# Performance work log

Hardware: AMD Instinct MI355X
Metric: run time of the kernel (lower is better)

## Reference

```python
import jax, jax.numpy as jnp
import numpy as np


def _gru_scan(xg, w_hh, b_hh, h0):
    """Scan a GRU (PyTorch gate order r,z,n) over time. xg: (T,B,3H) precomputed input projections."""
    def step(h, g):
        gh = h @ w_hh.T + b_hh
        i_r, i_z, i_n = jnp.split(g, 3, axis=-1)
        h_r, h_z, h_n = jnp.split(gh, 3, axis=-1)
        r = jax.nn.sigmoid(i_r + h_r)
        z = jax.nn.sigmoid(i_z + h_z)
        n = jnp.tanh(i_n + r * h_n)
        h_new = (1.0 - z) * n + z * h
        return h_new, h_new
    _, ys = jax.lax.scan(step, h0, xg)
    return ys  # (T, B, H)


def setup_inputs() -> dict:
    key = jax.random.key(0)
    ks = jax.random.split(key, 13)
    B, M, T = 64, 80, 2000
    C, H, K = 256, 256, 5
    s = 0.1
    return {
        "x": jax.random.normal(ks[0], (B, M, T), jnp.float32),
        "conv_w": jax.random.normal(ks[1], (C, M, K), jnp.float32) * s,
        "conv_b": jax.random.normal(ks[2], (C,), jnp.float32) * s,
        "w_ih_f": jax.random.normal(ks[3], (3 * H, C), jnp.float32) * s,
        "w_hh_f": jax.random.normal(ks[4], (3 * H, H), jnp.float32) * s,
        "b_ih_f": jax.random.normal(ks[5], (3 * H,), jnp.float32) * s,
        "b_hh_f": jax.random.normal(ks[6], (3 * H,), jnp.float32) * s,
        "w_ih_r": jax.random.normal(ks[7], (3 * H, C), jnp.float32) * s,
        "w_hh_r": jax.random.normal(ks[8], (3 * H, H), jnp.float32) * s,
        "b_ih_r": jax.random.normal(ks[9], (3 * H,), jnp.float32) * s,
        "b_hh_r": jax.random.normal(ks[10], (3 * H,), jnp.float32) * s,
        "clf_w": jax.random.normal(ks[11], (2, 2 * H), jnp.float32) * s,
        "clf_b": jax.random.normal(ks[12], (2,), jnp.float32) * s,
        "window_size": 100,
    }


def reference(x, conv_w, conv_b, w_ih_f, w_hh_f, b_ih_f, b_hh_f,
              w_ih_r, w_hh_r, b_ih_r, b_hh_r, clf_w, clf_b, window_size):
    # Streaming (inference_mode) branch of KWSNet, expressed incrementally:
    # per-step sliding-window conv == full valid conv; the 'bidirectional' GRU
    # with seq_len=1 per step and carried hidden == two independent GRUs both
    # scanned forward in time (one with the _reverse weight set).
    B = x.shape[0]
    K = conv_w.shape[-1]
    H = w_hh_f.shape[-1]
    # Conv1d valid + ReLU: (B, C, Tc), Tc = T - K + 1
    y = jax.lax.conv_general_dilated(x, conv_w, (1,), 'VALID',
                                     dimension_numbers=('NCH', 'OIH', 'NCH'))
    y = jax.nn.relu(y + conv_b[None, :, None])
    seq = jnp.transpose(y, (2, 0, 1))  # (Tc, B, C)
    h0 = jnp.zeros((B, H), seq.dtype)
    xg_f = seq @ w_ih_f.T + b_ih_f  # (Tc, B, 3H)
    xg_r = seq @ w_ih_r.T + b_ih_r
    enc = jnp.concatenate([
        _gru_scan(xg_f, w_hh_f, b_hh_f, h0),
        _gru_scan(xg_r, w_hh_r, b_hh_r, h0),
    ], axis=-1)  # (Tc, B, 2H)
    # Sliding mean over the last W encoder outputs (W = window_size - K + 1)
    W = window_size - K + 1
    cs = jnp.concatenate([jnp.zeros_like(enc[:1]), jnp.cumsum(enc, axis=0)], axis=0)
    means = (cs[W:] - cs[:-W]) / W  # (Tout, B, 2H), Tout = T - window_size + 1
    out = means @ clf_w.T + clf_b  # (Tout, B, 2)
    # torch stacks per-step (1, B, 2) outputs -> (Tout, 1, B, 2)
    return out[:, None, :, :]
```

## Files before the change

### kernel.cpp

```cpp
#include <hip/hip_runtime.h>
#include <hip/hip_bf16.h>


#define TT    2000
#define TC    1996
#define NB    64
#define MCH   80
#define NN    1536
#define TOUT  1901
#define TCH   126
#define NCHK  16
#define NRG   9
#define CROWS (TCH * NB)

typedef _Float16 h8_t __attribute__((ext_vector_type(8)));
typedef float    f4_t __attribute__((ext_vector_type(4)));

#define WQSCALE 254.0f
#define INV8    (1.0f / (254.0f * 127.0f))

#define OFF_SEQC ((size_t)0)
#define OFF_XG   ((size_t)8257536)
#define OFF_WT   ((size_t)57802752)
#define OFF_WCAT ((size_t)58212352)
#define OFF_HST  ((size_t)58998784)
#define OFF_WQ   ((size_t)59129856)
#define OFF_PS2  ((size_t)59523072)

__global__ void prep_kernel(const float* __restrict__ conv_w,
                            const float* __restrict__ wihf,
                            const float* __restrict__ wihr,
                            const float* __restrict__ whhf,
                            const float* __restrict__ whhr,
                            float* __restrict__ wT,
                            _Float16* __restrict__ wcat,
                            unsigned* __restrict__ wq) {
    int idx = blockIdx.x * 256 + threadIdx.x;
    if (idx < 400 * 256) {
        int c = idx & 255, mk = idx >> 8;
        wT[idx] = conv_w[c * 400 + mk];
    }
    int i2 = idx - 400 * 256;
    if (i2 >= 0 && i2 < NN * 256) {
        int k = i2 & 255, n = i2 >> 8;
        float v = (n < 768) ? wihf[n * 256 + k] : wihr[(n - 768) * 256 + k];
        wcat[i2] = (_Float16)v;
    }
    int i4 = idx - (400 * 256 + NN * 256);
    if (i4 >= 0 && i4 < 2 * 3 * 256 * 64) {
        int r  = i4 & 255;
        int j  = (i4 >> 8) & 63;
        int dg = i4 >> 14;
        const float* whh = (dg >= 3) ? whhr : whhf;
        int g = (dg >= 3) ? dg - 3 : dg;
        const float* wp = whh + (size_t)(g * 256 + r) * 256 + 4 * j;
        unsigned v = 0;
#pragma unroll
        for (int kk = 0; kk < 4; ++kk) {
            float q = rintf(wp[kk] * WQSCALE);
            q = fminf(fmaxf(q, -127.f), 127.f);
            v |= ((unsigned)((int)q & 0xFF)) << (8 * kk);
        }
        wq[((size_t)dg * 256 + r) * 64 + j] = v;
    }
}

#define SD4(a, b, c) __builtin_amdgcn_sdot4((int)(a), (int)(b), (c), false)

__global__ __launch_bounds__(256)
void fat_kernel(
    int nscan, const _Float16* __restrict__ xg_s, const uint4* __restrict__ wq,
    const float* __restrict__ bhhf, const float* __restrict__ bhhr,
    const float* __restrict__ clfw, float* __restrict__ hstate,
    float* __restrict__ psum2, int t0s, int lens, int first,
    int nproj, const _Float16* __restrict__ seqc_p, const _Float16* __restrict__ wcat,
    const float* __restrict__ bihf, const float* __restrict__ bihr,
    _Float16* __restrict__ xg_p, int lenp,
    int nconv, const float* __restrict__ x, const float* __restrict__ wT,
    const float* __restrict__ conv_b, _Float16* __restrict__ seqc_c,
    int t0c, int lenc)
{
    __shared__ __align__(16) char smem[86016];
    int bid = blockIdx.x;
    int tid = threadIdx.x;

    if (bid < nscan) {
        int d = bid >> 6, b = bid & 63;
        int i = tid, lane = tid & 63, wv = tid >> 6;
        const float* bhh = d ? bhhr : bhhf;
        unsigned (*hq8)[64]  = (unsigned(*)[64])smem;
        float (*cwp)[4][2]   = (float(*)[4][2])(smem + 512);

        uint4 wa[16], wb[16], wc[16];
        {
            const uint4* pa = wq + ((size_t)(d * 3 + 0) * 256 + i) * 16;
            const uint4* pb = wq + ((size_t)(d * 3 + 1) * 256 + i) * 16;
            const uint4* pc = wq + ((size_t)(d * 3 + 2) * 256 + i) * 16;
#pragma unroll
            for (int k = 0; k < 16; ++k) { wa[k] = pa[k]; wb[k] = pb[k]; wc[k] = pc[k]; }
        }
        float bhr = bhh[i], bhz = bhh[256 + i], bhn = bhh[512 + i];
        float cw0 = clfw[d * 256 + i], cw1 = clfw[512 + d * 256 + i];
        float h = first ? 0.f : hstate[(size_t)bid * 256 + i];

        ((char*)&hq8[0][0])[i] = (char)(int)rintf(h * 127.f);
        __syncthreads();

        const _Float16* xgp = xg_s + (size_t)d * CROWS * 768 + (size_t)b * 768 + i;
        float xr = (float)xgp[0], xz = (float)xgp[256], xn = (float)xgp[512];
        xgp += (size_t)64 * 768;

        int cur = 0;
        for (int t = 0; t < lens; ++t) {
            float pxr = (float)xgp[0], pxz = (float)xgp[256], pxn = (float)xgp[512];
            xgp += (size_t)64 * 768;

            const uint4* hqp = (const uint4*)&hq8[cur][0];
            int i0 = 0, i1 = 0, i2 = 0;
#pragma unroll
            for (int k = 0; k < 16; ++k) {
                uint4 hv = hqp[k];
                i0 = SD4(wa[k].x, hv.x, i0); i0 = SD4(wa[k].y, hv.y, i0);
                i0 = SD4(wa[k].z, hv.z, i0); i0 = SD4(wa[k].w, hv.w, i0);
                i1 = SD4(wb[k].x, hv.x, i1); i1 = SD4(wb[k].y, hv.y, i1);
                i1 = SD4(wb[k].z, hv.z, i1); i1 = SD4(wb[k].w, hv.w, i1);
                i2 = SD4(wc[k].x, hv.x, i2); i2 = SD4(wc[k].y, hv.y, i2);
                i2 = SD4(wc[k].z, hv.z, i2); i2 = SD4(wc[k].w, hv.w, i2);
            }

            float hr = (float)i0 * INV8 + bhr;
            float hz = (float)i1 * INV8 + bhz;
            float hn = (float)i2 * INV8 + bhn;
            float rg = 1.f / (1.f + __expf(-(xr + hr)));
            float zg = 1.f / (1.f + __expf(-(xz + hz)));
            float xnr = xn + rg * hn;
            float nv = 1.f - 2.f / (__expf(2.f * xnr) + 1.f);
            h = (1.f - zg) * nv + zg * h;

            float s0 = cw0 * h, s1 = cw1 * h;
#pragma unroll
            for (int off = 32; off; off >>= 1) {
                s0 += __shfl_xor(s0, off, 64);
                s1 += __shfl_xor(s1, off, 64);
            }
            int nxt = cur ^ 1;
            ((char*)&hq8[nxt][0])[i] = (char)(int)rintf(h * 127.f);
            if (lane == 0) { cwp[nxt][wv][0] = s0; cwp[nxt][wv][1] = s1; }
            __syncthreads();
            if (i == 0) {
                float a0 = cwp[nxt][0][0] + cwp[nxt][1][0] + cwp[nxt][2][0] + cwp[nxt][3][0];
                float a1 = cwp[nxt][0][1] + cwp[nxt][1][1] + cwp[nxt][2][1] + cwp[nxt][3][1];
                float* pp = psum2 + (((size_t)d * TC + (t0s + t)) * 64 + b) * 2;
                pp[0] = a0; pp[1] = a1;
            }
            cur = nxt;
            xr = pxr; xz = pxz; xn = pxn;
        }
        hstate[(size_t)bid * 256 + i] = h;

    } else if (bid < nscan + nproj) {
        int pb = bid - nscan;
        int n0 = (pb % 12) * 128;
        int rg = pb / 12;
        int ntiles = lenp >> 1;
        _Float16 (*Bs)[264] = (_Float16(*)[264])smem;
        _Float16 (*As)[72]  = (_Float16(*)[72])(smem + 67584);
        int lane = tid & 63, wv = tid >> 6;
        int wr = wv >> 1, wcn = wv & 1;
        int fm = lane & 15, fq = lane >> 4;
        int r = tid >> 1, part = tid & 1;

        {
            const uint4* srcB = (const uint4*)&wcat[(size_t)(n0 + r) * 256 + part * 128];
            uint4* dstB = (uint4*)&Bs[r][part * 128];
#pragma unroll
            for (int q = 0; q < 16; ++q) dstB[q] = srcB[q];
        }

        for (int tIdx = rg; tIdx < ntiles; tIdx += NRG) {
            int row0 = tIdx * 128;
            f4_t acc[4][4];
#pragma unroll
            for (int mt = 0; mt < 4; ++mt)
#pragma unroll
                for (int nt = 0; nt < 4; ++nt) acc[mt][nt] = (f4_t){0.f, 0.f, 0.f, 0.f};

            for (int kc = 0; kc < 4; ++kc) {
                const uint4* srcA = (const uint4*)&seqc_p[(size_t)(row0 + r) * 256 + kc * 64 + part * 32];
                uint4* dstA = (uint4*)&As[r][part * 32];
                dstA[0] = srcA[0]; dstA[1] = srcA[1]; dstA[2] = srcA[2]; dstA[3] = srcA[3];
                __syncthreads();
#pragma unroll
                for (int ks = 0; ks < 64; ks += 32) {
                    h8_t af[4], bf[4];
#pragma unroll
                    for (int mt = 0; mt < 4; ++mt)
                        af[mt] = *(const h8_t*)&As[wr * 64 + mt * 16 + fm][ks + fq * 8];
#pragma unroll
                    for (int nt = 0; nt < 4; ++nt)
                        bf[nt] = *(const h8_t*)&Bs[wcn * 64 + nt * 16 + fm][kc * 64 + ks + fq * 8];
#pragma unroll
                    for (int mt = 0; mt < 4; ++mt)
#pragma unroll
                        for (int nt = 0; nt < 4; ++nt)
                            acc[mt][nt] = __builtin_amdgcn_mfma_f32_16x16x32_f16(
                                af[mt], bf[nt], acc[mt][nt], 0, 0, 0);
                }
                __syncthreads();
            }
#pragma unroll
            for (int nt = 0; nt < 4; ++nt) {
                int col = n0 + wcn * 64 + nt * 16 + fm;
                int d = (col < 768) ? 0 : 1;
                int j = col - d * 768;
                float bias = d ? bihr[j] : bihf[j];
                size_t obase = (size_t)d * CROWS * 768 + j;
#pragma unroll
                for (int mt = 0; mt < 4; ++mt) {
                    int row = row0 + wr * 64 + mt * 16 + fq * 4;
#pragma unroll
                    for (int rr = 0; rr < 4; ++rr)
                        xg_p[obase + (size_t)(row + rr) * 768] = (_Float16)(acc[mt][nt][rr] + bias);
                }
            }
        }

    } else {
        int cb = bid - nscan - nproj;
        int tile = cb >> 6;
        int b    = cb & 63;
        float (*xs)[68] = (float(*)[68])smem;
        for (int idx = tid; idx < MCH * 68; idx += 256) {
            int m = idx / 68, ii = idx - m * 68;
            int tt = t0c + tile * 64 + ii;
            xs[m][ii] = (tt < TT) ? x[(size_t)b * (MCH * TT) + m * TT + tt] : 0.f;
        }
        __syncthreads();
        int lane = tid & 63, tg = tid >> 6;
        float acc[4][16];
#pragma unroll
        for (int cq = 0; cq < 4; ++cq)
#pragma unroll
            for (int t = 0; t < 16; ++t) acc[cq][t] = 0.f;

        for (int m = 0; m < MCH; ++m) {
            float xr_[20];
#pragma unroll
            for (int q = 0; q < 5; ++q) {
                float4 v = *(const float4*)&xs[m][tg * 16 + q * 4];
                xr_[q * 4 + 0] = v.x; xr_[q * 4 + 1] = v.y;
                xr_[q * 4 + 2] = v.z; xr_[q * 4 + 3] = v.w;
            }
#pragma unroll
            for (int cq = 0; cq < 4; ++cq) {
                int c = lane + cq * 64;
                const float* wp = wT + (size_t)(m * 5) * 256 + c;
                float w0_ = wp[0], w1_ = wp[256], w2_ = wp[512], w3_ = wp[768], w4_ = wp[1024];
#pragma unroll
                for (int t = 0; t < 16; ++t)
                    acc[cq][t] += w0_ * xr_[t] + w1_ * xr_[t + 1] + w2_ * xr_[t + 2]
                                + w3_ * xr_[t + 3] + w4_ * xr_[t + 4];
            }
        }
#pragma unroll
        for (int cq = 0; cq < 4; ++cq) {
            int c = lane + cq * 64;
            float cb_ = conv_b[c];
            for (int t = 0; t < 16; ++t) {
                int tl = tile * 64 + tg * 16 + t;
                if (tl < lenc) {
                    float v = acc[cq][t] + cb_;
                    v = v > 0.f ? v : 0.f;
                    seqc_c[((size_t)tl * 64 + b) * 256 + c] = (_Float16)v;
                }
            }
        }
    }
}

__global__ void final_kernel(const float* __restrict__ psum2, const float* __restrict__ clf_b,
                             const int* __restrict__ win, float* __restrict__ out) {
    int idx = blockIdx.x * 256 + threadIdx.x;
    if (idx >= TOUT * 128) return;
    int c = idx & 1;
    int rem = idx >> 1;
    int b = rem & 63;
    int tau = rem >> 6;
    int W = win[0] - 5 + 1;
    const float* p0 = psum2;
    const float* p1 = psum2 + (size_t)TC * 64 * 2;
    float s = 0.f;
    for (int j = 0; j < W; ++j) {
        size_t o = ((size_t)(tau + j) * 64 + b) * 2 + c;
        s += p0[o] + p1[o];
    }
    out[idx] = s / (float)W + clf_b[c];
}

extern "C" void kernel_launch(void* const* d_in, const int* in_sizes, int n_in,
                              void* d_out, int out_size, void* d_ws, size_t ws_size,
                              hipStream_t stream) {
    const float* x      = (const float*)d_in[0];
    const float* conv_w = (const float*)d_in[1];
    const float* conv_b = (const float*)d_in[2];
    const float* w_ih_f = (const float*)d_in[3];
    const float* w_hh_f = (const float*)d_in[4];
    const float* b_ih_f = (const float*)d_in[5];
    const float* b_hh_f = (const float*)d_in[6];
    const float* w_ih_r = (const float*)d_in[7];
    const float* w_hh_r = (const float*)d_in[8];
    const float* b_ih_r = (const float*)d_in[9];
    const float* b_hh_r = (const float*)d_in[10];
    const float* clf_w  = (const float*)d_in[11];
    const float* clf_b  = (const float*)d_in[12];
    const int*   win    = (const int*)d_in[13];
    float* out = (float*)d_out;

    char* ws = (char*)d_ws;
    _Float16* seqc = (_Float16*)(ws + OFF_SEQC);
    _Float16* xg   = (_Float16*)(ws + OFF_XG);
    float*    wT   = (float*)(ws + OFF_WT);
    _Float16* wcat = (_Float16*)(ws + OFF_WCAT);
    float*    hst  = (float*)(ws + OFF_HST);
    const uint4* wqp = (const uint4*)(ws + OFF_WQ);
    unsigned* wq   = (unsigned*)(ws + OFF_WQ);
    float*    ps2  = (float*)(ws + OFF_PS2);

    const size_t XGP = (size_t)2 * CROWS * 768;
    const size_t SQP = (size_t)CROWS * 256;

    int prep_elems = 400 * 256 + NN * 256 + 2 * 3 * 256 * 64;
    prep_kernel<<<(prep_elems + 255) / 256, 256, 0, stream>>>(
        conv_w, w_ih_f, w_ih_r, w_hh_f, w_hh_r, wT, wcat, wq);

    auto lenk = [](int k) { return (k < NCHK - 1) ? TCH : (TC - (NCHK - 1) * TCH); };

    fat_kernel<<<128, 256, 0, stream>>>(
        0, xg, wqp, b_hh_f, b_hh_r, clf_w, hst, ps2, 0, 0, 0,
        0, seqc, wcat, b_ih_f, b_ih_r, xg, 0,
        128, x, wT, conv_b, seqc, 0, lenk(0));

    fat_kernel<<<12 * NRG + 128, 256, 0, stream>>>(
        0, xg, wqp, b_hh_f, b_hh_r, clf_w, hst, ps2, 0, 0, 0,
        12 * NRG, seqc, wcat, b_ih_f, b_ih_r, xg, lenk(0),
        128, x, wT, conv_b, seqc + SQP, TCH, lenk(1));

    for (int k = 0; k < NCHK; ++k) {
        int lens = lenk(k);
        int np = (k + 1 < NCHK) ? 12 * NRG : 0;
        int lp = (k + 1 < NCHK) ? lenk(k + 1) : 0;
        int nc = (k + 2 < NCHK) ? 128 : 0;
        fat_kernel<<<128 + np + nc, 256, 0, stream>>>(
            128, xg + (size_t)(k & 1) * XGP, wqp, b_hh_f, b_hh_r, clf_w, hst, ps2,
            k * TCH, lens, (k == 0) ? 1 : 0,
            np, seqc + (size_t)((k + 1) & 1) * SQP, wcat, b_ih_f, b_ih_r,
            xg + (size_t)((k + 1) & 1) * XGP, lp,
            nc, x, wT, conv_b, seqc + (size_t)(k & 1) * SQP,
            (k + 2) * TCH, (k + 2 < NCHK) ? lenk(k + 2) : 0);
    }

    final_kernel<<<(TOUT * 128 + 255) / 256, 256, 0, stream>>>(ps2, clf_b, win, out);
}
```

Measured before the change: 2.363 ms.

## Size time chunks from workspace budget and grid-stride conv tiles

```diff
diff --git a/kernel.cpp b/kernel.cpp
--- a/kernel.cpp
+++ b/kernel.cpp
@@ -8,24 +8,13 @@
 #define MCH   80
 #define NN    1536
 #define TOUT  1901
-#define TCH   126
-#define NCHK  16
 #define NRG   9
-#define CROWS (TCH * NB)
 
 typedef _Float16 h8_t __attribute__((ext_vector_type(8)));
 typedef float    f4_t __attribute__((ext_vector_type(4)));
 
 #define WQSCALE 254.0f
 #define INV8    (1.0f / (254.0f * 127.0f))
-
-#define OFF_SEQC ((size_t)0)
-#define OFF_XG   ((size_t)8257536)
-#define OFF_WT   ((size_t)57802752)
-#define OFF_WCAT ((size_t)58212352)
-#define OFF_HST  ((size_t)58998784)
-#define OFF_WQ   ((size_t)59129856)
-#define OFF_PS2  ((size_t)59523072)
 
 __global__ void prep_kernel(const float* __restrict__ conv_w,
                             const float* __restrict__ wihf,
@@ -69,6 +58,7 @@
 
 __global__ __launch_bounds__(256)
 void fat_kernel(
+    int crows,
     int nscan, const _Float16* __restrict__ xg_s, const uint4* __restrict__ wq,
     const float* __restrict__ bhhf, const float* __restrict__ bhhr,
     const float* __restrict__ clfw, float* __restrict__ hstate,
@@ -106,7 +96,7 @@
         ((char*)&hq8[0][0])[i] = (char)(int)rintf(h * 127.f);
         __syncthreads();
 
-        const _Float16* xgp = xg_s + (size_t)d * CROWS * 768 + (size_t)b * 768 + i;
+        const _Float16* xgp = xg_s + (size_t)d * crows * 768 + (size_t)b * 768 + i;
         float xr = (float)xgp[0], xz = (float)xgp[256], xn = (float)xgp[512];
         xgp += (size_t)64 * 768;
 
@@ -214,7 +204,7 @@
                 int d = (col < 768) ? 0 : 1;
                 int j = col - d * 768;
                 float bias = d ? bihr[j] : bihf[j];
-                size_t obase = (size_t)d * CROWS * 768 + j;
+                size_t obase = (size_t)d * crows * 768 + j;
 #pragma unroll
                 for (int mt = 0; mt < 4; ++mt) {
                     int row = row0 + wr * 64 + mt * 16 + fq * 4;
@@ -227,53 +217,57 @@
 
     } else {
         int cb = bid - nscan - nproj;
-        int tile = cb >> 6;
-        int b    = cb & 63;
+        int units = ((lenc + 63) >> 6) << 6;
         float (*xs)[68] = (float(*)[68])smem;
-        for (int idx = tid; idx < MCH * 68; idx += 256) {
-            int m = idx / 68, ii = idx - m * 68;
-            int tt = t0c + tile * 64 + ii;
-            xs[m][ii] = (tt < TT) ? x[(size_t)b * (MCH * TT) + m * TT + tt] : 0.f;
-        }
-        __syncthreads();
         int lane = tid & 63, tg = tid >> 6;
-        float acc[4][16];
-#pragma unroll
-        for (int cq = 0; cq < 4; ++cq)
-#pragma unroll
-            for (int t = 0; t < 16; ++t) acc[cq][t] = 0.f;
-
-        for (int m = 0; m < MCH; ++m) {
-            float xr_[20];
-#pragma unroll
-            for (int q = 0; q < 5; ++q) {
-                float4 v = *(const float4*)&xs[m][tg * 16 + q * 4];
-                xr_[q * 4 + 0] = v.x; xr_[q * 4 + 1] = v.y;
-                xr_[q * 4 + 2] = v.z; xr_[q * 4 + 3] = v.w;
+        for (int u = cb; u < units; u += nconv) {
+            int tile = u >> 6;
+            int b    = u & 63;
+            for (int idx = tid; idx < MCH * 68; idx += 256) {
+                int m = idx / 68, ii = idx - m * 68;
+                int tt = t0c + tile * 64 + ii;
+                xs[m][ii] = (tt < TT) ? x[(size_t)b * (MCH * TT) + m * TT + tt] : 0.f;
+            }
+            __syncthreads();
+            float acc[4][16];
+#pragma unroll
+            for (int cq = 0; cq < 4; ++cq)
+#pragma unroll
+                for (int t = 0; t < 16; ++t) acc[cq][t] = 0.f;
+
+            for (int m = 0; m < MCH; ++m) {
+                float xr_[20];
+#pragma unroll
+                for (int q = 0; q < 5; ++q) {
+                    float4 v = *(const float4*)&xs[m][tg * 16 + q * 4];
+                    xr_[q * 4 + 0] = v.x; xr_[q * 4 + 1] = v.y;
+                    xr_[q * 4 + 2] = v.z; xr_[q * 4 + 3] = v.w;
+                }
+#pragma unroll
+                for (int cq = 0; cq < 4; ++cq) {
+                    int c = lane + cq * 64;
+                    const float* wp = wT + (size_t)(m * 5) * 256 + c;
+                    float w0_ = wp[0], w1_ = wp[256], w2_ = wp[512], w3_ = wp[768], w4_ = wp[1024];
+#pragma unroll
+                    for (int t = 0; t < 16; ++t)
+                        acc[cq][t] += w0_ * xr_[t] + w1_ * xr_[t + 1] + w2_ * xr_[t + 2]
+                                    + w3_ * xr_[t + 3] + w4_ * xr_[t + 4];
+                }
             }
 #pragma unroll
             for (int cq = 0; cq < 4; ++cq) {
                 int c = lane + cq * 64;
-                const float* wp = wT + (size_t)(m * 5) * 256 + c;
-                float w0_ = wp[0], w1_ = wp[256], w2_ = wp[512], w3_ = wp[768], w4_ = wp[1024];
-#pragma unroll
-                for (int t = 0; t < 16; ++t)
-                    acc[cq][t] += w0_ * xr_[t] + w1_ * xr_[t + 1] + w2_ * xr_[t + 2]
-                                + w3_ * xr_[t + 3] + w4_ * xr_[t + 4];
-            }
-        }
-#pragma unroll
-        for (int cq = 0; cq < 4; ++cq) {
-            int c = lane + cq * 64;
-            float cb_ = conv_b[c];
-            for (int t = 0; t < 16; ++t) {
-                int tl = tile * 64 + tg * 16 + t;
-                if (tl < lenc) {
-                    float v = acc[cq][t] + cb_;
-                    v = v > 0.f ? v : 0.f;
-                    seqc_c[((size_t)tl * 64 + b) * 256 + c] = (_Float16)v;
-                }
-            }
+                float cb_ = conv_b[c];
+                for (int t = 0; t < 16; ++t) {
+                    int tl = tile * 64 + tg * 16 + t;
+                    if (tl < lenc) {
+                        float v = acc[cq][t] + cb_;
+                        v = v > 0.f ? v : 0.f;
+                        seqc_c[((size_t)tl * 64 + b) * 256 + c] = (_Float16)v;
+                    }
+                }
+            }
+            __syncthreads();
         }
     }
 }
@@ -316,47 +310,60 @@
     const int*   win    = (const int*)d_in[13];
     float* out = (float*)d_out;
 
+    const size_t FIXED_TAIL = 409600 + 786432 + 131072 + 393216 + 2043904;
+    size_t budget = (ws_size > FIXED_TAIL) ? (ws_size - FIXED_TAIL) : 0;
+    int tch = (int)(budget / 458752);
+    if (tch > 250) tch = 250;
+    if (tch < 64) tch = 64;
+    tch &= ~1;
+    int nchk = (TC + tch - 1) / tch;
+    int crows = tch * 64;
+
     char* ws = (char*)d_ws;
-    _Float16* seqc = (_Float16*)(ws + OFF_SEQC);
-    _Float16* xg   = (_Float16*)(ws + OFF_XG);
-    float*    wT   = (float*)(ws + OFF_WT);
-    _Float16* wcat = (_Float16*)(ws + OFF_WCAT);
-    float*    hst  = (float*)(ws + OFF_HST);
-    const uint4* wqp = (const uint4*)(ws + OFF_WQ);
-    unsigned* wq   = (unsigned*)(ws + OFF_WQ);
-    float*    ps2  = (float*)(ws + OFF_PS2);
-
-    const size_t XGP = (size_t)2 * CROWS * 768;
-    const size_t SQP = (size_t)CROWS * 256;
+    size_t off = 0;
+    _Float16* seqc = (_Float16*)(ws + off); off += (size_t)2 * crows * 256 * 2;
+    _Float16* xg   = (_Float16*)(ws + off); off += (size_t)2 * 2 * crows * 768 * 2;
+    float*    wT   = (float*)(ws + off);    off += 409600;
+    _Float16* wcat = (_Float16*)(ws + off); off += 786432;
+    float*    hst  = (float*)(ws + off);    off += 131072;
+    unsigned* wq   = (unsigned*)(ws + off);
+    const uint4* wqp = (const uint4*)(ws + off); off += 393216;
+    float*    ps2  = (float*)(ws + off);
+
+    const size_t XGP = (size_t)2 * crows * 768;
+    const size_t SQP = (size_t)crows * 256;
 
     int prep_elems = 400 * 256 + NN * 256 + 2 * 3 * 256 * 64;
     prep_kernel<<<(prep_elems + 255) / 256, 256, 0, stream>>>(
         conv_w, w_ih_f, w_ih_r, w_hh_f, w_hh_r, wT, wcat, wq);
 
-    auto lenk = [](int k) { return (k < NCHK - 1) ? TCH : (TC - (NCHK - 1) * TCH); };
+    auto lenk = [&](int k) { return (k < nchk - 1) ? tch : (TC - (nchk - 1) * tch); };
 
     fat_kernel<<<128, 256, 0, stream>>>(
+        crows,
         0, xg, wqp, b_hh_f, b_hh_r, clf_w, hst, ps2, 0, 0, 0,
         0, seqc, wcat, b_ih_f, b_ih_r, xg, 0,
         128, x, wT, conv_b, seqc, 0, lenk(0));
 
     fat_kernel<<<12 * NRG + 128, 256, 0, stream>>>(
+        crows,
         0, xg, wqp, b_hh_f, b_hh_r, clf_w, hst, ps2, 0, 0, 0,
         12 * NRG, seqc, wcat, b_ih_f, b_ih_r, xg, lenk(0),
-        128, x, wT, conv_b, seqc + SQP, TCH, lenk(1));
-
-    for (int k = 0; k < NCHK; ++k) {
+        128, x, wT, conv_b, seqc + SQP, tch, lenk(1));
+
+    for (int k = 0; k < nchk; ++k) {
         int lens = lenk(k);
-        int np = (k + 1 < NCHK) ? 12 * NRG : 0;
-        int lp = (k + 1 < NCHK) ? lenk(k + 1) : 0;
-        int nc = (k + 2 < NCHK) ? 128 : 0;
+        int np = (k + 1 < nchk) ? 12 * NRG : 0;
+        int lp = (k + 1 < nchk) ? lenk(k + 1) : 0;
+        int nc = (k + 2 < nchk) ? 128 : 0;
         fat_kernel<<<128 + np + nc, 256, 0, stream>>>(
+            crows,
             128, xg + (size_t)(k & 1) * XGP, wqp, b_hh_f, b_hh_r, clf_w, hst, ps2,
-            k * TCH, lens, (k == 0) ? 1 : 0,
+            k * tch, lens, (k == 0) ? 1 : 0,
             np, seqc + (size_t)((k + 1) & 1) * SQP, wcat, b_ih_f, b_ih_r,
             xg + (size_t)((k + 1) & 1) * XGP, lp,
             nc, x, wT, conv_b, seqc + (size_t)(k & 1) * SQP,
-            (k + 2) * TCH, (k + 2 < NCHK) ? lenk(k + 2) : 0);
+            (k + 2) * tch, (k + 2 < nchk) ? lenk(k + 2) : 0);
     }
 
     final_kernel<<<(TOUT * 128 + 255) / 256, 256, 0, stream>>>(ps2, clf_b, win, out);
```

Result: no change. 2.383 ms (+0.9%).

## Process two batch rows per GRU scan block and loop conv blocks

Applied to the files above, without the earlier changes.

```diff
diff --git a/kernel.cpp b/kernel.cpp
--- a/kernel.cpp
+++ b/kernel.cpp
@@ -85,11 +85,12 @@
     int tid = threadIdx.x;
 
     if (bid < nscan) {
-        int d = bid >> 6, b = bid & 63;
+        int d = bid >> 5, p = bid & 31;
+        int b0 = p * 2, b1 = p * 2 + 1;
         int i = tid, lane = tid & 63, wv = tid >> 6;
         const float* bhh = d ? bhhr : bhhf;
-        unsigned (*hq8)[64]  = (unsigned(*)[64])smem;
-        float (*cwp)[4][2]   = (float(*)[4][2])(smem + 512);
+        unsigned (*hq8)[2][64] = (unsigned(*)[2][64])smem;
+        float (*cwp)[4][2][2]  = (float(*)[4][2][2])(smem + 1024);
 
         uint4 wa[16], wb[16], wc[16];
         {
@@ -101,62 +102,93 @@
         }
         float bhr = bhh[i], bhz = bhh[256 + i], bhn = bhh[512 + i];
         float cw0 = clfw[d * 256 + i], cw1 = clfw[512 + d * 256 + i];
-        float h = first ? 0.f : hstate[(size_t)bid * 256 + i];
-
-        ((char*)&hq8[0][0])[i] = (char)(int)rintf(h * 127.f);
+        float h0 = first ? 0.f : hstate[(size_t)(d * 64 + b0) * 256 + i];
+        float h1 = first ? 0.f : hstate[(size_t)(d * 64 + b1) * 256 + i];
+
+        ((char*)&hq8[0][0][0])[i] = (char)(int)rintf(h0 * 127.f);
+        ((char*)&hq8[0][1][0])[i] = (char)(int)rintf(h1 * 127.f);
         __syncthreads();
 
-        const _Float16* xgp = xg_s + (size_t)d * CROWS * 768 + (size_t)b * 768 + i;
-        float xr = (float)xgp[0], xz = (float)xgp[256], xn = (float)xgp[512];
-        xgp += (size_t)64 * 768;
+        const _Float16* xgpA = xg_s + (size_t)d * CROWS * 768 + (size_t)b0 * 768 + i;
+        const _Float16* xgpB = xgpA + 768;
+        float xr0 = (float)xgpA[0], xz0 = (float)xgpA[256], xn0 = (float)xgpA[512];
+        float xr1 = (float)xgpB[0], xz1 = (float)xgpB[256], xn1 = (float)xgpB[512];
+        xgpA += (size_t)64 * 768; xgpB += (size_t)64 * 768;
 
         int cur = 0;
         for (int t = 0; t < lens; ++t) {
-            float pxr = (float)xgp[0], pxz = (float)xgp[256], pxn = (float)xgp[512];
-            xgp += (size_t)64 * 768;
-
-            const uint4* hqp = (const uint4*)&hq8[cur][0];
-            int i0 = 0, i1 = 0, i2 = 0;
+            float pr0 = (float)xgpA[0], pz0 = (float)xgpA[256], pn0 = (float)xgpA[512];
+            float pr1 = (float)xgpB[0], pz1 = (float)xgpB[256], pn1 = (float)xgpB[512];
+            xgpA += (size_t)64 * 768; xgpB += (size_t)64 * 768;
+
+            const uint4* hqpA = (const uint4*)&hq8[cur][0][0];
+            const uint4* hqpB = (const uint4*)&hq8[cur][1][0];
+            int i0a = 0, i1a = 0, i2a = 0, i0b = 0, i1b = 0, i2b = 0;
 #pragma unroll
             for (int k = 0; k < 16; ++k) {
-                uint4 hv = hqp[k];
-                i0 = SD4(wa[k].x, hv.x, i0); i0 = SD4(wa[k].y, hv.y, i0);
-                i0 = SD4(wa[k].z, hv.z, i0); i0 = SD4(wa[k].w, hv.w, i0);
-                i1 = SD4(wb[k].x, hv.x, i1); i1 = SD4(wb[k].y, hv.y, i1);
-                i1 = SD4(wb[k].z, hv.z, i1); i1 = SD4(wb[k].w, hv.w, i1);
-                i2 = SD4(wc[k].x, hv.x, i2); i2 = SD4(wc[k].y, hv.y, i2);
-                i2 = SD4(wc[k].z, hv.z, i2); i2 = SD4(wc[k].w, hv.w, i2);
-            }
-
-            float hr = (float)i0 * INV8 + bhr;
-            float hz = (float)i1 * INV8 + bhz;
-            float hn = (float)i2 * INV8 + bhn;
-            float rg = 1.f / (1.f + __expf(-(xr + hr)));
-            float zg = 1.f / (1.f + __expf(-(xz + hz)));
-            float xnr = xn + rg * hn;
-            float nv = 1.f - 2.f / (__expf(2.f * xnr) + 1.f);
-            h = (1.f - zg) * nv + zg * h;
-
-            float s0 = cw0 * h, s1 = cw1 * h;
+                uint4 hva = hqpA[k], hvb = hqpB[k];
+                i0a = SD4(wa[k].x, hva.x, i0a); i0a = SD4(wa[k].y, hva.y, i0a);
+                i0a = SD4(wa[k].z, hva.z, i0a); i0a = SD4(wa[k].w, hva.w, i0a);
+                i1a = SD4(wb[k].x, hva.x, i1a); i1a = SD4(wb[k].y, hva.y, i1a);
+                i1a = SD4(wb[k].z, hva.z, i1a); i1a = SD4(wb[k].w, hva.w, i1a);
+                i2a = SD4(wc[k].x, hva.x, i2a); i2a = SD4(wc[k].y, hva.y, i2a);
+                i2a = SD4(wc[k].z, hva.z, i2a); i2a = SD4(wc[k].w, hva.w, i2a);
+                i0b = SD4(wa[k].x, hvb.x, i0b); i0b = SD4(wa[k].y, hvb.y, i0b);
+                i0b = SD4(wa[k].z, hvb.z, i0b); i0b = SD4(wa[k].w, hvb.w, i0b);
+                i1b = SD4(wb[k].x, hvb.x, i1b); i1b = SD4(wb[k].y, hvb.y, i1b);
+                i1b = SD4(wb[k].z, hvb.z, i1b); i1b = SD4(wb[k].w, hvb.w, i1b);
+                i2b = SD4(wc[k].x, hvb.x, i2b); i2b = SD4(wc[k].y, hvb.y, i2b);
+                i2b = SD4(wc[k].z, hvb.z, i2b); i2b = SD4(wc[k].w, hvb.w, i2b);
+            }
+
+            float hr0 = (float)i0a * INV8 + bhr;
+            float hz0 = (float)i1a * INV8 + bhz;
+            float hn0 = (float)i2a * INV8 + bhn;
+            float rg0 = 1.f / (1.f + __expf(-(xr0 + hr0)));
+            float zg0 = 1.f / (1.f + __expf(-(xz0 + hz0)));
+            float nv0 = 1.f - 2.f / (__expf(2.f * (xn0 + rg0 * hn0)) + 1.f);
+            h0 = (1.f - zg0) * nv0 + zg0 * h0;
+
+            float hr1 = (float)i0b * INV8 + bhr;
+            float hz1 = (float)i1b * INV8 + bhz;
+            float hn1 = (float)i2b * INV8 + bhn;
+            float rg1 = 1.f / (1.f + __expf(-(xr1 + hr1)));
+            float zg1 = 1.f / (1.f + __expf(-(xz1 + hz1)));
+            float nv1 = 1.f - 2.f / (__expf(2.f * (xn1 + rg1 * hn1)) + 1.f);
+            h1 = (1.f - zg1) * nv1 + zg1 * h1;
+
+            float s0a = cw0 * h0, s1a = cw1 * h0;
+            float s0b = cw0 * h1, s1b = cw1 * h1;
 #pragma unroll
             for (int off = 32; off; off >>= 1) {
-                s0 += __shfl_xor(s0, off, 64);
-                s1 += __shfl_xor(s1, off, 64);
+                s0a += __shfl_xor(s0a, off, 64);
+                s1a += __shfl_xor(s1a, off, 64);
+                s0b += __shfl_xor(s0b, off, 64);
+                s1b += __shfl_xor(s1b, off, 64);
             }
             int nxt = cur ^ 1;
-            ((char*)&hq8[nxt][0])[i] = (char)(int)rintf(h * 127.f);
-            if (lane == 0) { cwp[nxt][wv][0] = s0; cwp[nxt][wv][1] = s1; }
+            ((char*)&hq8[nxt][0][0])[i] = (char)(int)rintf(h0 * 127.f);
+            ((char*)&hq8[nxt][1][0])[i] = (char)(int)rintf(h1 * 127.f);
+            if (lane == 0) {
+                cwp[nxt][wv][0][0] = s0a; cwp[nxt][wv][0][1] = s1a;
+                cwp[nxt][wv][1][0] = s0b; cwp[nxt][wv][1][1] = s1b;
+            }
             __syncthreads();
             if (i == 0) {
-                float a0 = cwp[nxt][0][0] + cwp[nxt][1][0] + cwp[nxt][2][0] + cwp[nxt][3][0];
-                float a1 = cwp[nxt][0][1] + cwp[nxt][1][1] + cwp[nxt][2][1] + cwp[nxt][3][1];
-                float* pp = psum2 + (((size_t)d * TC + (t0s + t)) * 64 + b) * 2;
-                pp[0] = a0; pp[1] = a1;
+                float a0 = cwp[nxt][0][0][0] + cwp[nxt][1][0][0] + cwp[nxt][2][0][0] + cwp[nxt][3][0][0];
+                float a1 = cwp[nxt][0][0][1] + cwp[nxt][1][0][1] + cwp[nxt][2][0][1] + cwp[nxt][3][0][1];
+                float c0 = cwp[nxt][0][1][0] + cwp[nxt][1][1][0] + cwp[nxt][2][1][0] + cwp[nxt][3][1][0];
+                float c1 = cwp[nxt][0][1][1] + cwp[nxt][1][1][1] + cwp[nxt][2][1][1] + cwp[nxt][3][1][1];
+                float* pp0 = psum2 + (((size_t)d * TC + (t0s + t)) * 64 + b0) * 2;
+                pp0[0] = a0; pp0[1] = a1;
+                pp0[2] = c0; pp0[3] = c1;
             }
             cur = nxt;
-            xr = pxr; xz = pxz; xn = pxn;
-        }
-        hstate[(size_t)bid * 256 + i] = h;
+            xr0 = pr0; xz0 = pz0; xn0 = pn0;
+            xr1 = pr1; xz1 = pz1; xn1 = pn1;
+        }
+        hstate[(size_t)(d * 64 + b0) * 256 + i] = h0;
+        hstate[(size_t)(d * 64 + b1) * 256 + i] = h1;
 
     } else if (bid < nscan + nproj) {
         int pb = bid - nscan;
@@ -227,53 +259,57 @@
 
     } else {
         int cb = bid - nscan - nproj;
-        int tile = cb >> 6;
-        int b    = cb & 63;
+        int units = ((lenc + 63) >> 6) << 6;
         float (*xs)[68] = (float(*)[68])smem;
-        for (int idx = tid; idx < MCH * 68; idx += 256) {
-            int m = idx / 68, ii = idx - m * 68;
-            int tt = t0c + tile * 64 + ii;
-            xs[m][ii] = (tt < TT) ? x[(size_t)b * (MCH * TT) + m * TT + tt] : 0.f;
-        }
-        __syncthreads();
         int lane = tid & 63, tg = tid >> 6;
-        float acc[4][16];
-#pragma unroll
-        for (int cq = 0; cq < 4; ++cq)
-#pragma unroll
-            for (int t = 0; t < 16; ++t) acc[cq][t] = 0.f;
-
-        for (int m = 0; m < MCH; ++m) {
-            float xr_[20];
-#pragma unroll
-            for (int q = 0; q < 5; ++q) {
-                float4 v = *(const float4*)&xs[m][tg * 16 + q * 4];
-                xr_[q * 4 + 0] = v.x; xr_[q * 4 + 1] = v.y;
-                xr_[q * 4 + 2] = v.z; xr_[q * 4 + 3] = v.w;
+        for (int u = cb; u < units; u += nconv) {
+            int tile = u >> 6;
+            int b    = u & 63;
+            for (int idx = tid; idx < MCH * 68; idx += 256) {
+                int m = idx / 68, ii = idx - m * 68;
+                int tt = t0c + tile * 64 + ii;
+                xs[m][ii] = (tt < TT) ? x[(size_t)b * (MCH * TT) + m * TT + tt] : 0.f;
+            }
+            __syncthreads();
+            float acc[4][16];
+#pragma unroll
+            for (int cq = 0; cq < 4; ++cq)
+#pragma unroll
+                for (int t = 0; t < 16; ++t) acc[cq][t] = 0.f;
+
+            for (int m = 0; m < MCH; ++m) {
+                float xr_[20];
+#pragma unroll
+                for (int q = 0; q < 5; ++q) {
+                    float4 v = *(const float4*)&xs[m][tg * 16 + q * 4];
+                    xr_[q * 4 + 0] = v.x; xr_[q * 4 + 1] = v.y;
+                    xr_[q * 4 + 2] = v.z; xr_[q * 4 + 3] = v.w;
+                }
+#pragma unroll
+                for (int cq = 0; cq < 4; ++cq) {
+                    int c = lane + cq * 64;
+                    const float* wp = wT + (size_t)(m * 5) * 256 + c;
+                    float w0_ = wp[0], w1_ = wp[256], w2_ = wp[512], w3_ = wp[768], w4_ = wp[1024];
+#pragma unroll
+                    for (int t = 0; t < 16; ++t)
+                        acc[cq][t] += w0_ * xr_[t] + w1_ * xr_[t + 1] + w2_ * xr_[t + 2]
+                                    + w3_ * xr_[t + 3] + w4_ * xr_[t + 4];
+                }
             }
 #pragma unroll
             for (int cq = 0; cq < 4; ++cq) {
                 int c = lane + cq * 64;
-                const float* wp = wT + (size_t)(m * 5) * 256 + c;
-                float w0_ = wp[0], w1_ = wp[256], w2_ = wp[512], w3_ = wp[768], w4_ = wp[1024];
-#pragma unroll
-                for (int t = 0; t < 16; ++t)
-                    acc[cq][t] += w0_ * xr_[t] + w1_ * xr_[t + 1] + w2_ * xr_[t + 2]
-                                + w3_ * xr_[t + 3] + w4_ * xr_[t + 4];
-            }
-        }
-#pragma unroll
-        for (int cq = 0; cq < 4; ++cq) {
-            int c = lane + cq * 64;
-            float cb_ = conv_b[c];
-            for (int t = 0; t < 16; ++t) {
-                int tl = tile * 64 + tg * 16 + t;
-                if (tl < lenc) {
-                    float v = acc[cq][t] + cb_;
-                    v = v > 0.f ? v : 0.f;
-                    seqc_c[((size_t)tl * 64 + b) * 256 + c] = (_Float16)v;
-                }
-            }
+                float cb_ = conv_b[c];
+                for (int t = 0; t < 16; ++t) {
+                    int tl = tile * 64 + tg * 16 + t;
+                    if (tl < lenc) {
+                        float v = acc[cq][t] + cb_;
+                        v = v > 0.f ? v : 0.f;
+                        seqc_c[((size_t)tl * 64 + b) * 256 + c] = (_Float16)v;
+                    }
+                }
+            }
+            __syncthreads();
         }
     }
 }
@@ -349,9 +385,9 @@
         int lens = lenk(k);
         int np = (k + 1 < NCHK) ? 12 * NRG : 0;
         int lp = (k + 1 < NCHK) ? lenk(k + 1) : 0;
-        int nc = (k + 2 < NCHK) ? 128 : 0;
-        fat_kernel<<<128 + np + nc, 256, 0, stream>>>(
-            128, xg + (size_t)(k & 1) * XGP, wqp, b_hh_f, b_hh_r, clf_w, hst, ps2,
+        int nc = (k + 2 < NCHK) ? 84 : 0;
+        fat_kernel<<<64 + np + nc, 256, 0, stream>>>(
+            64, xg + (size_t)(k & 1) * XGP, wqp, b_hh_f, b_hh_r, clf_w, hst, ps2,
             k * TCH, lens, (k == 0) ? 1 : 0,
             np, seqc + (size_t)((k + 1) & 1) * SQP, wcat, b_ih_f, b_ih_r,
             xg + (size_t)((k + 1) & 1) * XGP, lp,
```

Result: slower. 3.800 ms (+60.8%).
